# Kernel tuning notes

Hardware: AMD Instinct MI355X
Metric: run time of the kernel (lower is better)

The kernel has to match this reference:

```python
import jax, jax.numpy as jnp
import numpy as np
from itertools import product

B, D, H, W_, C = 2, 64, 64, 64, 96
OUT = 192  # c_multiplier * dim
EPS = 1e-5


def setup_inputs() -> dict:
    key = jax.random.key(0)
    k1, k2 = jax.random.split(key)
    x = jax.random.normal(k1, (B, D, H, W_, C), dtype=jnp.float32)
    ln_w = jnp.ones((8 * C,), dtype=jnp.float32)
    ln_b = jnp.zeros((8 * C,), dtype=jnp.float32)
    W = jax.random.normal(k2, (OUT, 8 * C), dtype=jnp.float32) * 0.02
    return {"x": x, "ln_w": ln_w, "ln_b": ln_b, "W": W}


def reference(x, ln_w, ln_b, W):
    # strided patch gather + concat: order matches itertools.product over (0,1)^3
    parts = [x[:, s0::2, s1::2, s2::2, :] for s0, s1, s2 in product((0, 1), repeat=3)]
    y = jnp.concatenate(parts, axis=-1)  # [B, D/2, H/2, W/2, 8C]
    # LayerNorm over last dim
    mu = jnp.mean(y, axis=-1, keepdims=True)
    var = jnp.mean(jnp.square(y - mu), axis=-1, keepdims=True)
    y = (y - mu) * jax.lax.rsqrt(var + EPS) * ln_w + ln_b
    # linear reduction (bias=False); torch Linear weight is [out, in]
    return jnp.einsum('bdhwc,oc->bdhwo', y, W)
```

## Files before the change

### kernel.cpp

```cpp
#include <hip/hip_runtime.h>
#include <stdint.h>

#define C_IN   96
#define KIN    768
#define NOUT   192
#define EPS    1e-5f
#define NKIT   24

typedef __bf16 bf16x8 __attribute__((ext_vector_type(8)));
typedef float  f32x4  __attribute__((ext_vector_type(4)));

static __device__ __forceinline__ unsigned int f2bf(float f) {
    union { float f; unsigned int u; } v; v.f = f;
    return (v.u + 0x7fffu + ((v.u >> 16) & 1u)) >> 16;
}
static __device__ __forceinline__ float bf2f(unsigned int s) {
    union { unsigned int u; float f; } v; v.u = s << 16;
    return v.f;
}
static __device__ __forceinline__ int swz(int a) {
    return a ^ (((a >> 8) & 7) << 4);
}

__global__ __launch_bounds__(256) void prep_bias(
    const float* __restrict__ W, const float* __restrict__ lnw,
    const float* __restrict__ lnb, float* __restrict__ bias,
    float* __restrict__ Scol)
{
    int o = blockIdx.x;
    int tid = threadIdx.x;
    float bpart = 0.f, spart = 0.f;
    for (int c = tid; c < KIN; c += 256) {
        float w = W[(size_t)o * KIN + c];
        spart += bf2f(f2bf(w * lnw[c]));
        bpart += w * lnb[c];
    }
    #pragma unroll
    for (int m = 32; m >= 1; m >>= 1) {
        bpart += __shfl_xor(bpart, m, 64);
        spart += __shfl_xor(spart, m, 64);
    }
    __shared__ float redb[4], reds[4];
    if ((tid & 63) == 0) { redb[tid >> 6] = bpart; reds[tid >> 6] = spart; }
    __syncthreads();
    if (tid == 0) {
        bias[o] = redb[0] + redb[1] + redb[2] + redb[3];
        Scol[o] = reds[0] + reds[1] + reds[2] + reds[3];
    }
}

__global__ __launch_bounds__(256) void prep_swz(
    const float* __restrict__ W, const float* __restrict__ lnw,
    unsigned short* __restrict__ Wsw)
{
    const int nt = blockIdx.x;
    for (int s = threadIdx.x; s < NKIT * 64; s += 256) {
        const int kk = s >> 6;
        const int l  = s & 63;
        const int row = nt * 16 + (l & 15);
        const int k0  = kk * 32 + (l >> 4) * 8;
        const float* src = W + (size_t)row * KIN + k0;
        unsigned int p[4];
        #pragma unroll
        for (int j = 0; j < 4; ++j) {
            float a = src[2 * j]     * lnw[k0 + 2 * j];
            float b = src[2 * j + 1] * lnw[k0 + 2 * j + 1];
            p[j] = f2bf(a) | (f2bf(b) << 16);
        }
        *(uint4*)&Wsw[(size_t)((nt * NKIT + kk) * 64 + l) * 8] =
            make_uint4(p[0], p[1], p[2], p[3]);
    }
}

__global__ __launch_bounds__(256) void repack_kernel(
    const float* __restrict__ x, unsigned short* __restrict__ yt,
    float2* __restrict__ stats)
{
    __shared__ unsigned char tile[24576 + 64];

    const int tid = threadIdx.x;
    const int mt  = blockIdx.x;
    const int b  = mt >> 11;
    const int d  = (mt >> 6) & 31;
    const int h  = (mt >> 1) & 31;
    const int wh = mt & 1;

    const int r = tid >> 6;
    const int l = tid & 63;
    const int s0 = r >> 1, s1 = r & 1;
    const float* src = x +
        (((size_t)(b * 64 + 2 * d + s0) * 64 + (2 * h + s1)) * 64 + wh * 32) * C_IN
        + l * 4;

    float4 v[12];
    #pragma unroll
    for (int it = 0; it < 12; ++it)
        v[it] = *(const float4*)(src + it * 256);
    __builtin_amdgcn_sched_barrier(0);

    #pragma unroll
    for (int it = 0; it < 12; ++it) {
        const int p  = it * 256 + l * 4;
        const int t5 = p >> 5;
        const int xw = (t5 * 171) >> 9;
        const int c  = p - xw * 96;
        const int m  = xw >> 1;
        const int k  = (r * 2 + (xw & 1)) * 96 + c;
        const int kk = k >> 5, quad = (k >> 3) & 3, sub = (k & 4) << 1;
        const int addr = ((kk << 6) + m + (quad << 4)) * 16 + sub;
        uint2 pk;
        pk.x = f2bf(v[it].x) | (f2bf(v[it].y) << 16);
        pk.y = f2bf(v[it].z) | (f2bf(v[it].w) << 16);
        *(uint2*)(tile + swz(addr)) = pk;
    }
    __syncthreads();

    char* dst = (char*)yt + (size_t)mt * 24576;
    #pragma unroll
    for (int s = 0; s < 6; ++s) {
        const int lin = s * 4096 + tid * 16;
        *(uint4*)(dst + lin) = *(const uint4*)(tile + swz(lin));
    }

    {
        const int m = tid >> 4, j = tid & 15;
        float sum = 0.f, sq = 0.f;
        #pragma unroll
        for (int e6 = 0; e6 < 6; ++e6) {
            const int e  = j + e6 * 16;
            const int kk = e >> 2, quad = e & 3;
            const int a  = ((kk << 6) + m + (quad << 4)) * 16;
            uint4 u = *(const uint4*)(tile + swz(a));
            const unsigned int w[4] = {u.x, u.y, u.z, u.w};
            #pragma unroll
            for (int q = 0; q < 4; ++q) {
                float lo = bf2f(w[q] & 0xffffu);
                float hi = bf2f(w[q] >> 16);
                sum += lo + hi;
                sq  += lo * lo + hi * hi;
            }
        }
        #pragma unroll
        for (int msk = 1; msk <= 8; msk <<= 1) {
            sum += __shfl_xor(sum, msk, 16);
            sq  += __shfl_xor(sq,  msk, 16);
        }
        if (j == 0) {
            float mean = sum * (1.f / 768.f);
            float var  = sq * (1.f / 768.f) - mean * mean;
            stats[mt * 16 + m] = make_float2(mean, rsqrtf(var + EPS));
        }
    }
}

__global__ __launch_bounds__(256, 3) void gemm_kernel(
    const unsigned short* __restrict__ yt, const unsigned short* __restrict__ Wsw,
    const float* __restrict__ bias, const float* __restrict__ Scol,
    const float2* __restrict__ stats, float* __restrict__ out)
{
    const int tid  = threadIdx.x;
    const int wv   = tid >> 6;
    const int l    = tid & 63;
    const int l15  = l & 15;
    const int quad = l >> 4;
    const int nh   = wv & 1;
    const int mt0  = blockIdx.x * 4 + (wv >> 1) * 2;

    const char* aptr0 = (const char*)yt + (size_t)mt0 * 24576 + l * 16;
    const char* aptr1 = aptr0 + 24576;
    const char* bptr  = (const char*)Wsw + (size_t)nh * 6 * NKIT * 1024 + l * 16;

    f32x4 acc[2][6];
    #pragma unroll
    for (int mi = 0; mi < 2; ++mi)
        #pragma unroll
        for (int nt = 0; nt < 6; ++nt)
            acc[mi][nt] = (f32x4){0.f, 0.f, 0.f, 0.f};

    bf16x8 A[2][2], Bv[2][6];
    #pragma unroll
    for (int p = 0; p < 2; ++p) {
        A[p][0] = *(const bf16x8*)(aptr0 + p * 1024);
        A[p][1] = *(const bf16x8*)(aptr1 + p * 1024);
        #pragma unroll
        for (int nt = 0; nt < 6; ++nt)
            Bv[p][nt] = *(const bf16x8*)(bptr + (size_t)(nt * NKIT + p) * 1024);
    }
    #pragma unroll
    for (int kk = 0; kk < NKIT; ++kk) {
        const int c = kk & 1;
        bf16x8 nA0, nA1, nB[6];
        if (kk < NKIT - 2) {
            const int k2 = kk + 2;
            nA0 = *(const bf16x8*)(aptr0 + k2 * 1024);
            nA1 = *(const bf16x8*)(aptr1 + k2 * 1024);
            #pragma unroll
            for (int nt = 0; nt < 6; ++nt)
                nB[nt] = *(const bf16x8*)(bptr + (size_t)(nt * NKIT + k2) * 1024);
        }
        #pragma unroll
        for (int nt = 0; nt < 6; ++nt) {
            acc[0][nt] = __builtin_amdgcn_mfma_f32_16x16x32_bf16(A[c][0], Bv[c][nt], acc[0][nt], 0, 0, 0);
            acc[1][nt] = __builtin_amdgcn_mfma_f32_16x16x32_bf16(A[c][1], Bv[c][nt], acc[1][nt], 0, 0, 0);
        }
        if (kk < NKIT - 2) {
            A[c][0] = nA0; A[c][1] = nA1;
            #pragma unroll
            for (int nt = 0; nt < 6; ++nt) Bv[c][nt] = nB[nt];
        }
    }

    float2 st[2][4];
    #pragma unroll
    for (int mi = 0; mi < 2; ++mi)
        #pragma unroll
        for (int rr = 0; rr < 4; ++rr)
            st[mi][rr] = stats[(mt0 + mi) * 16 + quad * 4 + rr];

    #pragma unroll
    for (int nt = 0; nt < 6; ++nt) {
        const int col = nh * 96 + nt * 16 + l15;
        const float S = Scol[col];
        const float bc = bias[col];
        #pragma unroll
        for (int mi = 0; mi < 2; ++mi) {
            #pragma unroll
            for (int rr = 0; rr < 4; ++rr) {
                const int t = (mt0 + mi) * 16 + quad * 4 + rr;
                const float mu = st[mi][rr].x, rs = st[mi][rr].y;
                out[(size_t)t * NOUT + col] = rs * acc[mi][nt][rr] - rs * mu * S + bc;
            }
        }
    }
}

extern "C" void kernel_launch(void* const* d_in, const int* in_sizes, int n_in,
                              void* d_out, int out_size, void* d_ws, size_t ws_size,
                              hipStream_t stream) {
    const float* x   = (const float*)d_in[0];
    const float* lnw = (const float*)d_in[1];
    const float* lnb = (const float*)d_in[2];
    const float* W   = (const float*)d_in[3];
    float* out = (float*)d_out;

    char* ws = (char*)d_ws;
    unsigned short* Wsw  = (unsigned short*)ws;
    float* bias          = (float*)(ws + 294912);
    float* Scol          = (float*)(ws + 295680);
    float2* stats        = (float2*)(ws + 296448);
    unsigned short* yt   = (unsigned short*)(ws + 1048576);

    prep_bias<<<NOUT, 256, 0, stream>>>(W, lnw, lnb, bias, Scol);
    prep_swz<<<12, 256, 0, stream>>>(W, lnw, Wsw);
    repack_kernel<<<4096, 256, 0, stream>>>(x, yt, stats);
    gemm_kernel<<<1024, 256, 0, stream>>>(yt, Wsw, bias, Scol, stats, out);
}
```

Measured before the change: 399.7 us.

## Fuse repack and GEMM into one kernel using LDS tile as A operand

Merges the patch-gather/LayerNorm-stats kernel with the GEMM so each block converts its 16 tokens to bf16 in LDS and immediately multiplies them against the prepped weights. This removes writing and re-reading the bf16 intermediate and the stats buffer through global memory. In exchange each block streams the full weight matrix for only 16 rows, raising L2 traffic for B, and per-block MFMA reuse is lower.

New measurement: 332.5 us. 1.2x faster.

```diff
diff --git a/kernel.cpp b/kernel.cpp
--- a/kernel.cpp
+++ b/kernel.cpp
@@ -72,18 +72,20 @@
     }
 }
 
-__global__ __launch_bounds__(256) void repack_kernel(
-    const float* __restrict__ x, unsigned short* __restrict__ yt,
-    float2* __restrict__ stats)
+__global__ __launch_bounds__(256, 6) void merge_kernel(
+    const float* __restrict__ x, const unsigned short* __restrict__ Wsw,
+    const float* __restrict__ bias, const float* __restrict__ Scol,
+    float* __restrict__ out)
 {
     __shared__ unsigned char tile[24576 + 64];
+    __shared__ float muL[16], rsL[16];
 
     const int tid = threadIdx.x;
     const int mt  = blockIdx.x;
-    const int b  = mt >> 11;
-    const int d  = (mt >> 6) & 31;
-    const int h  = (mt >> 1) & 31;
-    const int wh = mt & 1;
+    const int b   = mt >> 11;
+    const int d   = (mt >> 6) & 31;
+    const int h   = (mt >> 1) & 31;
+    const int wh  = mt & 1;
 
     const int r = tid >> 6;
     const int l = tid & 63;
@@ -115,21 +117,14 @@
     }
     __syncthreads();
 
-    char* dst = (char*)yt + (size_t)mt * 24576;
-    #pragma unroll
-    for (int s = 0; s < 6; ++s) {
-        const int lin = s * 4096 + tid * 16;
-        *(uint4*)(dst + lin) = *(const uint4*)(tile + swz(lin));
-    }
-
     {
-        const int m = tid >> 4, j = tid & 15;
+        const int sm = tid >> 4, j = tid & 15;
         float sum = 0.f, sq = 0.f;
         #pragma unroll
-        for (int e6 = 0; e6 < 6; ++e6) {
-            const int e  = j + e6 * 16;
-            const int kk = e >> 2, quad = e & 3;
-            const int a  = ((kk << 6) + m + (quad << 4)) * 16;
+        for (int t = 0; t < 6; ++t) {
+            const int e  = j + t * 16;
+            const int akk = e >> 2, aq = e & 3;
+            const int a  = ((akk << 6) + sm + (aq << 4)) * 16;
             uint4 u = *(const uint4*)(tile + swz(a));
             const unsigned int w[4] = {u.x, u.y, u.z, u.w};
             #pragma unroll
@@ -148,88 +143,57 @@
         if (j == 0) {
             float mean = sum * (1.f / 768.f);
             float var  = sq * (1.f / 768.f) - mean * mean;
-            stats[mt * 16 + m] = make_float2(mean, rsqrtf(var + EPS));
-        }
-    }
-}
-
-__global__ __launch_bounds__(256, 3) void gemm_kernel(
-    const unsigned short* __restrict__ yt, const unsigned short* __restrict__ Wsw,
-    const float* __restrict__ bias, const float* __restrict__ Scol,
-    const float2* __restrict__ stats, float* __restrict__ out)
-{
-    const int tid  = threadIdx.x;
-    const int wv   = tid >> 6;
-    const int l    = tid & 63;
-    const int l15  = l & 15;
-    const int quad = l >> 4;
-    const int nh   = wv & 1;
-    const int mt0  = blockIdx.x * 4 + (wv >> 1) * 2;
-
-    const char* aptr0 = (const char*)yt + (size_t)mt0 * 24576 + l * 16;
-    const char* aptr1 = aptr0 + 24576;
-    const char* bptr  = (const char*)Wsw + (size_t)nh * 6 * NKIT * 1024 + l * 16;
-
-    f32x4 acc[2][6];
-    #pragma unroll
-    for (int mi = 0; mi < 2; ++mi)
-        #pragma unroll
-        for (int nt = 0; nt < 6; ++nt)
-            acc[mi][nt] = (f32x4){0.f, 0.f, 0.f, 0.f};
-
-    bf16x8 A[2][2], Bv[2][6];
+            muL[sm] = mean;
+            rsL[sm] = rsqrtf(var + EPS);
+        }
+    }
+    __syncthreads();
+
+    const int m15 = l & 15;
+    const int qd  = l >> 4;
+    const char* bp = (const char*)Wsw + ((size_t)(3 * r) * NKIT * 64 + l) * 16;
+
+    f32x4 acc0 = {0.f, 0.f, 0.f, 0.f};
+    f32x4 acc1 = {0.f, 0.f, 0.f, 0.f};
+    f32x4 acc2 = {0.f, 0.f, 0.f, 0.f};
+
+    bf16x8 A[2], B0[2], B1[2], B2[2];
     #pragma unroll
     for (int p = 0; p < 2; ++p) {
-        A[p][0] = *(const bf16x8*)(aptr0 + p * 1024);
-        A[p][1] = *(const bf16x8*)(aptr1 + p * 1024);
-        #pragma unroll
-        for (int nt = 0; nt < 6; ++nt)
-            Bv[p][nt] = *(const bf16x8*)(bptr + (size_t)(nt * NKIT + p) * 1024);
+        A[p]  = *(const bf16x8*)(tile + swz((p * 64 + l) * 16));
+        B0[p] = *(const bf16x8*)(bp + (size_t)p * 1024);
+        B1[p] = *(const bf16x8*)(bp + 24576 + (size_t)p * 1024);
+        B2[p] = *(const bf16x8*)(bp + 49152 + (size_t)p * 1024);
     }
     #pragma unroll
     for (int kk = 0; kk < NKIT; ++kk) {
         const int c = kk & 1;
-        bf16x8 nA0, nA1, nB[6];
+        bf16x8 nA, nB0, nB1, nB2;
         if (kk < NKIT - 2) {
             const int k2 = kk + 2;
-            nA0 = *(const bf16x8*)(aptr0 + k2 * 1024);
-            nA1 = *(const bf16x8*)(aptr1 + k2 * 1024);
-            #pragma unroll
-            for (int nt = 0; nt < 6; ++nt)
-                nB[nt] = *(const bf16x8*)(bptr + (size_t)(nt * NKIT + k2) * 1024);
-        }
-        #pragma unroll
-        for (int nt = 0; nt < 6; ++nt) {
-            acc[0][nt] = __builtin_amdgcn_mfma_f32_16x16x32_bf16(A[c][0], Bv[c][nt], acc[0][nt], 0, 0, 0);
-            acc[1][nt] = __builtin_amdgcn_mfma_f32_16x16x32_bf16(A[c][1], Bv[c][nt], acc[1][nt], 0, 0, 0);
-        }
-        if (kk < NKIT - 2) {
-            A[c][0] = nA0; A[c][1] = nA1;
-            #pragma unroll
-            for (int nt = 0; nt < 6; ++nt) Bv[c][nt] = nB[nt];
-        }
-    }
-
-    float2 st[2][4];
-    #pragma unroll
-    for (int mi = 0; mi < 2; ++mi)
-        #pragma unroll
-        for (int rr = 0; rr < 4; ++rr)
-            st[mi][rr] = stats[(mt0 + mi) * 16 + quad * 4 + rr];
-
-    #pragma unroll
-    for (int nt = 0; nt < 6; ++nt) {
-        const int col = nh * 96 + nt * 16 + l15;
-        const float S = Scol[col];
+            nA  = *(const bf16x8*)(tile + swz((k2 * 64 + l) * 16));
+            nB0 = *(const bf16x8*)(bp + (size_t)k2 * 1024);
+            nB1 = *(const bf16x8*)(bp + 24576 + (size_t)k2 * 1024);
+            nB2 = *(const bf16x8*)(bp + 49152 + (size_t)k2 * 1024);
+        }
+        acc0 = __builtin_amdgcn_mfma_f32_16x16x32_bf16(A[c], B0[c], acc0, 0, 0, 0);
+        acc1 = __builtin_amdgcn_mfma_f32_16x16x32_bf16(A[c], B1[c], acc1, 0, 0, 0);
+        acc2 = __builtin_amdgcn_mfma_f32_16x16x32_bf16(A[c], B2[c], acc2, 0, 0, 0);
+        if (kk < NKIT - 2) { A[c] = nA; B0[c] = nB0; B1[c] = nB1; B2[c] = nB2; }
+    }
+
+    const int nb = r * 48;
+    #pragma unroll
+    for (int nt = 0; nt < 3; ++nt) {
+        const int col = nb + nt * 16 + m15;
+        const float S  = Scol[col];
         const float bc = bias[col];
-        #pragma unroll
-        for (int mi = 0; mi < 2; ++mi) {
-            #pragma unroll
-            for (int rr = 0; rr < 4; ++rr) {
-                const int t = (mt0 + mi) * 16 + quad * 4 + rr;
-                const float mu = st[mi][rr].x, rs = st[mi][rr].y;
-                out[(size_t)t * NOUT + col] = rs * acc[mi][nt][rr] - rs * mu * S + bc;
-            }
+        const f32x4 av = (nt == 0) ? acc0 : (nt == 1) ? acc1 : acc2;
+        #pragma unroll
+        for (int rr = 0; rr < 4; ++rr) {
+            const int row = qd * 4 + rr;
+            const float rs = rsL[row], mu = muL[row];
+            out[((size_t)mt * 16 + row) * NOUT + col] = rs * av[rr] - rs * mu * S + bc;
         }
     }
 }
@@ -244,14 +208,11 @@
     float* out = (float*)d_out;
 
     char* ws = (char*)d_ws;
-    unsigned short* Wsw  = (unsigned short*)ws;
-    float* bias          = (float*)(ws + 294912);
-    float* Scol          = (float*)(ws + 295680);
-    float2* stats        = (float2*)(ws + 296448);
-    unsigned short* yt   = (unsigned short*)(ws + 1048576);
+    unsigned short* Wsw = (unsigned short*)ws;
+    float* bias         = (float*)(ws + 294912);
+    float* Scol         = (float*)(ws + 295680);
 
     prep_bias<<<NOUT, 256, 0, stream>>>(W, lnw, lnb, bias, Scol);
     prep_swz<<<12, 256, 0, stream>>>(W, lnw, Wsw);
-    repack_kernel<<<4096, 256, 0, stream>>>(x, yt, stats);
-    gemm_kernel<<<1024, 256, 0, stream>>>(yt, Wsw, bias, Scol, stats, out);
-}
+    merge_kernel<<<4096, 256, 0, stream>>>(x, Wsw, bias, Scol, out);
+}
```
